# Performance work log

Hardware: AMD Instinct MI355X
Metric: run time of the kernel (lower is better)

Reference implementation:

```python
import jax, jax.numpy as jnp
import numpy as np

N_NODES = 100000


def _gcn_norm(edge_index, num_nodes):
    """Add self-loops and compute symmetric GCN normalization coefficients.
    Returns (src, dst, norm) for the augmented edge list."""
    loop = jnp.arange(num_nodes, dtype=edge_index.dtype)
    src = jnp.concatenate([edge_index[0], loop])
    dst = jnp.concatenate([edge_index[1], loop])
    deg = jax.ops.segment_sum(jnp.ones_like(src, dtype=jnp.float32), dst,
                              num_segments=num_nodes)
    dinv = jnp.where(deg > 0, jax.lax.rsqrt(deg), 0.0)
    norm = dinv[src] * dinv[dst]  # [E + N]
    return src, dst, norm


def setup_inputs() -> dict:
    key = jax.random.key(0)
    ks = jax.random.split(key, 7)
    d = 64
    E = 1000000
    x = jax.random.normal(ks[0], (N_NODES, d), dtype=jnp.float32)
    edge_index = jax.random.randint(ks[1], (2, E), 0, N_NODES, dtype=jnp.int64)
    s = 1.0 / np.sqrt(d)
    Ws = jax.random.normal(ks[2], (3, d, d), dtype=jnp.float32) * s
    bs = jax.random.normal(ks[3], (3, d), dtype=jnp.float32) * 0.02
    W_out = jax.random.normal(ks[4], (d, d), dtype=jnp.float32) * s
    b_out = jax.random.normal(ks[5], (d,), dtype=jnp.float32) * 0.02
    return {"x": x, "edge_index": edge_index, "Ws": Ws, "bs": bs,
            "W_out": W_out, "b_out": b_out}


def reference(x, edge_index, Ws, bs, W_out, b_out):
    num_nodes = x.shape[0]
    src, dst, norm = _gcn_norm(edge_index, num_nodes)  # fixed graph -> compute once
    for i in range(Ws.shape[0]):  # small fixed layer count
        h = x @ Ws[i]                              # [N, d] linear transform
        msg = norm[:, None] * h[src]               # gather + scale  [E+N, d]
        x = jax.ops.segment_sum(msg, dst, num_segments=num_nodes) + bs[i]
        x = jax.nn.relu(x)
    return x @ W_out + b_out
```

## Files before the change

### kernel.cpp

```cpp
#include <hip/hip_runtime.h>
#include <hip/hip_bf16.h>

#define D 64
#define BSHIFT 8
#define BNODES 256
#define BCAP 4096
#define PTILE 2048

typedef __attribute__((ext_vector_type(8))) short short8;
typedef __attribute__((ext_vector_type(4))) float float4v;


__device__ __forceinline__ float bf16u_to_f32(unsigned short u) {
  union { unsigned int i; float f; } c;
  c.i = ((unsigned int)u) << 16;
  return c.f;
}

__device__ __forceinline__ unsigned short f32_to_bf16u(float f) {
  union { float f; unsigned int u; } c;
  c.f = f;
  unsigned int r = (c.u + 0x7fffu + ((c.u >> 16) & 1u)) >> 16;
  return (unsigned short)r;
}


__global__ void k_probe(const void* W, const void* ei, int* flags) {
  int lane = threadIdx.x & 63;
  const unsigned short* wb = (const unsigned short*)W;
  bool big = false;
  for (int i = lane; i < 512; i += 64) {
    float v = bf16u_to_f32(wb[i]);
    if (!(fabsf(v) < 100.f)) big = true;
  }
  int anybig = __any(big);
  const int* e32 = (const int*)ei;
  bool nz = (e32[2 * lane + 1] != 0);
  int anynz = __any(nz);
  if (threadIdx.x == 0) {
    flags[0] = anybig ? 1 : 0;
    flags[1] = anynz ? 0 : 1;
  }
}


__global__ __launch_bounds__(256) void k_prep(
    const void* __restrict__ Ws, const void* __restrict__ Wout,
    const void* __restrict__ bs, const void* __restrict__ bout,
    const int* __restrict__ flags, unsigned short* __restrict__ WT,
    float* __restrict__ biasf, int* __restrict__ bucket_cursor) {
  int f32 = flags[0];
  int gid = blockIdx.x * 256 + threadIdx.x;
  int stride = gridDim.x * 256;

  for (int i = gid; i < 512; i += stride) bucket_cursor[i] = i * BCAP;

  for (int i = gid; i < 4 * 4096; i += stride) {
    int l = i >> 12;
    int r = i & 4095;
    int k = r >> 6;
    int nn = r & 63;
    unsigned short v;
    if (l < 3) {
      v = f32 ? f32_to_bf16u(((const float*)Ws)[l * 4096 + r])
              : ((const unsigned short*)Ws)[l * 4096 + r];
    } else {
      v = f32 ? f32_to_bf16u(((const float*)Wout)[r])
              : ((const unsigned short*)Wout)[r];
    }
    WT[l * 4096 + nn * 64 + k] = v;
  }
  for (int i = gid; i < 4 * 64; i += stride) {
    int l = i >> 6;
    int j = i & 63;
    float v;
    if (l < 3)
      v = f32 ? ((const float*)bs)[l * 64 + j]
              : bf16u_to_f32(((const unsigned short*)bs)[l * 64 + j]);
    else
      v = f32 ? ((const float*)bout)[j]
              : bf16u_to_f32(((const unsigned short*)bout)[j]);
    biasf[i] = v;
  }
}


__global__ __launch_bounds__(256) void k_partition(
    const void* __restrict__ ei, const int* __restrict__ flags,
    int* __restrict__ bucket_cursor, int* __restrict__ packed, int e) {
  __shared__ int lhist[512];
  __shared__ int lbase[512];
  int tid = threadIdx.x;
  int t0 = blockIdx.x * PTILE;
  int tend = min(t0 + PTILE, e);
  if (t0 >= e) return;
  int i64 = flags[1];

  for (int b = tid; b < 512; b += 256) lhist[b] = 0;
  __syncthreads();

  if (i64) {
    const long long* dst = (const long long*)ei + e;
    for (int i = t0 + tid; i < tend; i += 256)
      atomicAdd(&lhist[((int)dst[i]) >> BSHIFT], 1);
  } else {
    const int* dst = (const int*)ei + e;
    for (int i = t0 + tid; i < tend; i += 256)
      atomicAdd(&lhist[dst[i] >> BSHIFT], 1);
  }
  __syncthreads();

  for (int b = tid; b < 512; b += 256) {
    int c = lhist[b];
    lbase[b] = c ? atomicAdd(&bucket_cursor[b], c) : 0;
    lhist[b] = 0;
  }
  __syncthreads();

  if (i64) {
    const long long* srcp = (const long long*)ei;
    const long long* dstp = srcp + e;
    for (int i = t0 + tid; i < tend; i += 256) {
      int s = (int)srcp[i];
      int d = (int)dstp[i];
      int b = d >> BSHIFT;
      int r = atomicAdd(&lhist[b], 1);
      packed[lbase[b] + r] = (s << BSHIFT) | (d & (BNODES - 1));
    }
  } else {
    const int* srcp = (const int*)ei;
    const int* dstp = srcp + e;
    for (int i = t0 + tid; i < tend; i += 256) {
      int s = srcp[i];
      int d = dstp[i];
      int b = d >> BSHIFT;
      int r = atomicAdd(&lhist[b], 1);
      packed[lbase[b] + r] = (s << BSHIFT) | (d & (BNODES - 1));
    }
  }
}

__global__ __launch_bounds__(256) void k_sort_csr(
    const int* __restrict__ packed, const int* __restrict__ bucket_cursor,
    int* __restrict__ csr, int2* __restrict__ rowrange,
    float* __restrict__ dinv, int n) {
  __shared__ int lcnt[BNODES];
  __shared__ int lofs[BNODES];
  __shared__ int sbuf[BNODES];
  int tid = threadIdx.x;
  int bucket = blockIdx.x;
  int node0 = bucket << BSHIFT;
  int nodes = min(BNODES, n - node0);
  int s0 = bucket * BCAP;
  int s1 = bucket_cursor[bucket];
  lcnt[tid] = 0;
  __syncthreads();
  for (int i = s0 + tid; i < s1; i += 256)
    atomicAdd(&lcnt[packed[i] & (BNODES - 1)], 1);
  __syncthreads();
  int v = lcnt[tid];
  sbuf[tid] = v;
  __syncthreads();
  for (int off = 1; off < BNODES; off <<= 1) {
    int tv = (tid >= off) ? sbuf[tid - off] : 0;
    __syncthreads();
    sbuf[tid] += tv;
    __syncthreads();
  }
  int excl = sbuf[tid] - v;
  lofs[tid] = excl;
  lcnt[tid] = 0;
  if (tid < nodes) {
    rowrange[node0 + tid] = make_int2(s0 + excl, s0 + excl + v);
    dinv[node0 + tid] = rsqrtf((float)(v + 1));
  }
  __syncthreads();
  for (int i = s0 + tid; i < s1; i += 256) {
    int pk = packed[i];
    int ld = pk & (BNODES - 1);
    int r = atomicAdd(&lcnt[ld], 1);
    csr[s0 + lofs[ld] + r] = pk >> BSHIFT;
  }
}


__global__ __launch_bounds__(256) void k_scale(
    const void* __restrict__ x0, const int* __restrict__ flags,
    const float* __restrict__ dinv, ushort4* __restrict__ z, int n16) {
  int f32 = flags[0];
  int i = blockIdx.x * 256 + threadIdx.x;
  int stride = gridDim.x * 256;
  for (; i < n16; i += stride) {
    float d = dinv[i >> 4];
    ushort4 o;
    if (f32) {
      float4 v = ((const float4*)x0)[i];
      o.x = f32_to_bf16u(d * v.x);
      o.y = f32_to_bf16u(d * v.y);
      o.z = f32_to_bf16u(d * v.z);
      o.w = f32_to_bf16u(d * v.w);
    } else {
      ushort4 v = ((const ushort4*)x0)[i];
      o.x = f32_to_bf16u(d * bf16u_to_f32(v.x));
      o.y = f32_to_bf16u(d * bf16u_to_f32(v.y));
      o.z = f32_to_bf16u(d * bf16u_to_f32(v.z));
      o.w = f32_to_bf16u(d * bf16u_to_f32(v.w));
    }
    z[i] = o;
  }
}

__global__ __launch_bounds__(256, 4) void k_fused(
    const unsigned short* __restrict__ z, const int2* __restrict__ rowrange,
    const int* __restrict__ csr, const float* __restrict__ dinv,
    const unsigned short* __restrict__ WT, const float* __restrict__ biasf,
    unsigned short* __restrict__ out, int n, int scale_out) {
  __shared__ unsigned short ybf[16 * 80];
  int tid = threadIdx.x;
  int lane = tid & 63;
  int w = tid >> 6;
  int q = lane >> 4;
  int f = lane & 15;

  short8 b0 = *(const short8*)(WT + (size_t)(f + 16 * w) * 64 + q * 8);
  short8 b1 = *(const short8*)(WT + (size_t)(f + 16 * w) * 64 + 32 + q * 8);

  int row0 = blockIdx.x * 16;
  int base_node = row0 + w * 4;
  const ushort4* z4 = (const ushort4*)z;

  int2 rr[4];
#pragma unroll
  for (int j = 0; j < 4; j++) rr[j] = rowrange[base_node + j];

  float ac[4][4];
#pragma unroll
  for (int j = 0; j < 4; j++) {
    ushort4 sv = z4[(size_t)(base_node + j) * 16 + f];
    ac[j][0] = (q == 0) ? bf16u_to_f32(sv.x) : 0.f;
    ac[j][1] = (q == 0) ? bf16u_to_f32(sv.y) : 0.f;
    ac[j][2] = (q == 0) ? bf16u_to_f32(sv.z) : 0.f;
    ac[j][3] = (q == 0) ? bf16u_to_f32(sv.w) : 0.f;
  }

  int srcs[16];
  bool mm[16];
#pragma unroll
  for (int j = 0; j < 4; j++) {
#pragma unroll
    for (int u = 0; u < 4; u++) {
      int i = rr[j].x + 4 * u + q;
      bool m = i < rr[j].y;
      mm[j * 4 + u] = m;
      srcs[j * 4 + u] = csr[m ? i : rr[j].x];
    }
  }
  ushort4 g[16];
#pragma unroll
  for (int t = 0; t < 16; t++) g[t] = z4[(size_t)srcs[t] * 16 + f];
#pragma unroll
  for (int j = 0; j < 4; j++) {
#pragma unroll
    for (int u = 0; u < 4; u++) {
      ushort4 v = g[j * 4 + u];
      if (mm[j * 4 + u]) {
        ac[j][0] += bf16u_to_f32(v.x);
        ac[j][1] += bf16u_to_f32(v.y);
        ac[j][2] += bf16u_to_f32(v.z);
        ac[j][3] += bf16u_to_f32(v.w);
      }
    }
  }

#pragma unroll
  for (int j = 0; j < 4; j++) {
    for (int base = rr[j].x + 16; base < rr[j].y; base += 16) {
      int ts[4];
      bool tm[4];
#pragma unroll
      for (int u = 0; u < 4; u++) {
        int i = base + 4 * u + q;
        tm[u] = i < rr[j].y;
        ts[u] = csr[tm[u] ? i : rr[j].x];
      }
      ushort4 tv[4];
#pragma unroll
      for (int u = 0; u < 4; u++) tv[u] = z4[(size_t)ts[u] * 16 + f];
#pragma unroll
      for (int u = 0; u < 4; u++) {
        if (tm[u]) {
          ac[j][0] += bf16u_to_f32(tv[u].x);
          ac[j][1] += bf16u_to_f32(tv[u].y);
          ac[j][2] += bf16u_to_f32(tv[u].z);
          ac[j][3] += bf16u_to_f32(tv[u].w);
        }
      }
    }
  }

#pragma unroll
  for (int j = 0; j < 4; j++) {
#pragma unroll
    for (int c = 0; c < 4; c++) {
      ac[j][c] += __shfl_xor(ac[j][c], 16, 64);
      ac[j][c] += __shfl_xor(ac[j][c], 32, 64);
    }
  }
  if (q == 0) {
#pragma unroll
    for (int j = 0; j < 4; j++) {
      float dv = dinv[base_node + j];
      ushort4 o;
      o.x = f32_to_bf16u(dv * ac[j][0]);
      o.y = f32_to_bf16u(dv * ac[j][1]);
      o.z = f32_to_bf16u(dv * ac[j][2]);
      o.w = f32_to_bf16u(dv * ac[j][3]);
      *(ushort4*)&ybf[(w * 4 + j) * 80 + 4 * f] = o;
    }
  }
  __syncthreads();

  short8 a0 = *(const short8*)&ybf[f * 80 + q * 8];
  short8 a1 = *(const short8*)&ybf[f * 80 + 32 + q * 8];
  float4v zz = {0.f, 0.f, 0.f, 0.f};
  float4v acc = __builtin_amdgcn_mfma_f32_16x16x32_bf16(a0, b0, zz, 0, 0, 0);
  acc = __builtin_amdgcn_mfma_f32_16x16x32_bf16(a1, b1, acc, 0, 0, 0);

  float bv = biasf[16 * w + f];
  if (scale_out) {
    float4 dv4 = *(const float4*)(dinv + row0 + q * 4);
    float d[4] = {dv4.x, dv4.y, dv4.z, dv4.w};
#pragma unroll
    for (int reg = 0; reg < 4; reg++) {
      int row = row0 + q * 4 + reg;
      if (row < n)
        out[(size_t)row * 64 + 16 * w + f] =
            f32_to_bf16u(d[reg] * fmaxf(acc[reg] + bv, 0.f));
    }
  } else {
#pragma unroll
    for (int reg = 0; reg < 4; reg++) {
      int row = row0 + q * 4 + reg;
      if (row < n)
        out[(size_t)row * 64 + 16 * w + f] =
            f32_to_bf16u(fmaxf(acc[reg] + bv, 0.f));
    }
  }
}

__global__ __launch_bounds__(256) void k_gemm_final(
    const unsigned short* __restrict__ xin,
    const unsigned short* __restrict__ WT, const float* __restrict__ bias,
    void* __restrict__ out, const int* __restrict__ flags, int ntiles) {
  int lane = threadIdx.x & 63;
  int wid = threadIdx.x >> 6;
  int f = lane & 15;
  int q = lane >> 4;

  short8 bfr[4][2];
#pragma unroll
  for (int ct = 0; ct < 4; ct++)
#pragma unroll
    for (int kt = 0; kt < 2; kt++)
      bfr[ct][kt] =
          *(const short8*)(WT + (size_t)(f + 16 * ct) * 64 + kt * 32 + q * 8);

  int wave = blockIdx.x * 4 + wid;
  int nwaves = gridDim.x * 4;
  for (int t = wave; t < ntiles; t += nwaves) {
    int row0 = t * 16;
    const unsigned short* xr = xin + (size_t)(row0 + f) * 64 + q * 8;
    short8 a0 = *(const short8*)(xr);
    short8 a1 = *(const short8*)(xr + 32);
    float4v acc[4];
#pragma unroll
    for (int ct = 0; ct < 4; ct++) {
      float4v z = {0.f, 0.f, 0.f, 0.f};
      acc[ct] =
          __builtin_amdgcn_mfma_f32_16x16x32_bf16(a0, bfr[ct][0], z, 0, 0, 0);
      acc[ct] = __builtin_amdgcn_mfma_f32_16x16x32_bf16(a1, bfr[ct][1],
                                                        acc[ct], 0, 0, 0);
    }
    int f32o = flags[0];
    float bv[4];
#pragma unroll
    for (int ct = 0; ct < 4; ct++) bv[ct] = bias[f + 16 * ct];
    if (f32o) {
      float* op = (float*)out;
#pragma unroll
      for (int reg = 0; reg < 4; reg++) {
        size_t rb = (size_t)(row0 + q * 4 + reg) * 64 + f;
#pragma unroll
        for (int ct = 0; ct < 4; ct++) op[rb + 16 * ct] = acc[ct][reg] + bv[ct];
      }
    } else {
      unsigned short* op = (unsigned short*)out;
#pragma unroll
      for (int reg = 0; reg < 4; reg++) {
        size_t rb = (size_t)(row0 + q * 4 + reg) * 64 + f;
#pragma unroll
        for (int ct = 0; ct < 4; ct++)
          op[rb + 16 * ct] = f32_to_bf16u(acc[ct][reg] + bv[ct]);
      }
    }
  }
}


extern "C" void kernel_launch(void* const* d_in, const int* in_sizes, int n_in,
                              void* d_out, int out_size, void* d_ws,
                              size_t ws_size, hipStream_t stream) {
  const void* x0 = d_in[0];
  const void* ei = d_in[1];
  const void* Ws = d_in[2];
  const void* bs = d_in[3];
  const void* Wout = d_in[4];
  const void* bout = d_in[5];

  const int N = in_sizes[0] / D;
  const int E = in_sizes[1] / 2;
  const int NBUC = (N + BNODES - 1) >> BSHIFT;
  const int NT = (N + 15) / 16;

  char* p = (char*)d_ws;
  auto alloc = [&](size_t bytes) {
    char* r = p;
    p += (bytes + 511) & ~(size_t)511;
    return r;
  };
  int* flags = (int*)alloc(8);
  int* bucket_cursor = (int*)alloc(512 * 4);
  int* packed = (int*)alloc((size_t)512 * BCAP * 4);
  int* csr = (int*)alloc((size_t)512 * BCAP * 4);
  int2* rowrange = (int2*)alloc((size_t)N * 8);
  float* dinv = (float*)alloc((size_t)N * 4);
  unsigned short* WT = (unsigned short*)alloc(4 * 4096 * 2);
  float* biasf = (float*)alloc(4 * 64 * 4);
  unsigned short* za = (unsigned short*)alloc((size_t)N * D * 2);
  unsigned short* zb = (unsigned short*)alloc((size_t)N * D * 2);
  (void)ws_size;
  (void)n_in;
  (void)out_size;

  k_probe<<<1, 64, 0, stream>>>(Ws, ei, flags);
  k_prep<<<32, 256, 0, stream>>>(Ws, Wout, bs, bout, flags, WT, biasf,
                                 bucket_cursor);
  int ptiles = (E + PTILE - 1) / PTILE;
  k_partition<<<ptiles, 256, 0, stream>>>(ei, flags, bucket_cursor, packed, E);
  k_sort_csr<<<NBUC, 256, 0, stream>>>(packed, bucket_cursor, csr, rowrange,
                                       dinv, N);
  k_scale<<<1024, 256, 0, stream>>>(x0, flags, dinv, (ushort4*)za, N * 16);

  k_fused<<<NT, 256, 0, stream>>>(za, rowrange, csr, dinv, WT + 0 * 4096,
                                  biasf + 0 * 64, zb, N, 1);
  k_fused<<<NT, 256, 0, stream>>>(zb, rowrange, csr, dinv, WT + 1 * 4096,
                                  biasf + 1 * 64, za, N, 1);
  k_fused<<<NT, 256, 0, stream>>>(za, rowrange, csr, dinv, WT + 2 * 4096,
                                  biasf + 2 * 64, zb, N, 0);
  k_gemm_final<<<(NT + 3) / 4, 256, 0, stream>>>(zb, WT + 3 * 4096,
                                                 biasf + 3 * 64, d_out, flags,
                                                 NT);
}
```

Before: 264.7 us.

## Gather neighbor rows with 16-byte loads and shuffle-broadcast CSR indices

Reworks the fused gather-aggregate kernel so each lane loads 8 bf16 features (short8) rather than 4. Eight lanes now cover a 64-wide row, so each wave gathers 8 neighbors per instruction. Row ranges and CSR indices are loaded once per wave and broadcast with shuffles. The self-loop is folded into slot 0 of the first 16-entry batch. This is meant to cut the number of memory instructions and redundant index loads, at the cost of more registers (four 8-float accumulators) and a three-stage cross-lane reduction.

Measured after the change: 243.6 us. -8.0%, faster.

```diff
diff --git a/kernel.cpp b/kernel.cpp
--- a/kernel.cpp
+++ b/kernel.cpp
@@ -221,110 +221,123 @@
   int w = tid >> 6;
   int q = lane >> 4;
   int f = lane & 15;
+  int h = lane & 7;
+  int g8 = lane >> 3;
 
   short8 b0 = *(const short8*)(WT + (size_t)(f + 16 * w) * 64 + q * 8);
   short8 b1 = *(const short8*)(WT + (size_t)(f + 16 * w) * 64 + 32 + q * 8);
 
   int row0 = blockIdx.x * 16;
   int base_node = row0 + w * 4;
-  const ushort4* z4 = (const ushort4*)z;
-
-  int2 rr[4];
-#pragma unroll
-  for (int j = 0; j < 4; j++) rr[j] = rowrange[base_node + j];
-
-  float ac[4][4];
+  const short8* z8 = (const short8*)z;
+
+  int rrw = 0;
+  if (lane < 8) rrw = ((const int*)rowrange)[(size_t)base_node * 2 + lane];
+  int rx0 = __shfl(rrw, 0, 64);
+  int ry0 = __shfl(rrw, 1, 64);
+  int rx1 = __shfl(rrw, 2, 64);
+  int ry1 = __shfl(rrw, 3, 64);
+  int rx2 = __shfl(rrw, 4, 64);
+  int ry2 = __shfl(rrw, 5, 64);
+  int rx3 = __shfl(rrw, 6, 64);
+  int ry3 = __shfl(rrw, 7, 64);
+  int deg0 = ry0 - rx0;
+  int deg1 = ry1 - rx1;
+  int deg2 = ry2 - rx2;
+  int deg3 = ry3 - rx3;
+
+  int jx = lane >> 4;
+  int m = lane & 15;
+  int rxj = (jx & 2) ? ((jx & 1) ? rx3 : rx2) : ((jx & 1) ? rx1 : rx0);
+  int dgj = (jx & 2) ? ((jx & 1) ? deg3 : deg2) : ((jx & 1) ? deg1 : deg0);
+  int coff = (m >= 1 && m <= dgj) ? (m - 1) : 0;
+  int idx = csr[rxj + coff];
+  if (m == 0) idx = base_node + jx;
+
+  float ac[4][4][2];
+  float a0[8] = {0, 0, 0, 0, 0, 0, 0, 0};
+  float a1[8] = {0, 0, 0, 0, 0, 0, 0, 0};
+  float a2[8] = {0, 0, 0, 0, 0, 0, 0, 0};
+  float a3[8] = {0, 0, 0, 0, 0, 0, 0, 0};
+  (void)ac;
+
+  short8 g[8];
+#pragma unroll
+  for (int t = 0; t < 8; t++) {
+    int u = ((t & 1) << 3) + g8;
+    int sl = ((t >> 1) << 4) + u;
+    int s = __shfl(idx, sl, 64);
+    g[t] = z8[(size_t)s * 8 + h];
+  }
+#pragma unroll
+  for (int t = 0; t < 8; t++) {
+    int u = ((t & 1) << 3) + g8;
+    const int j = t >> 1;
+    int dg = (j == 0) ? deg0 : (j == 1) ? deg1 : (j == 2) ? deg2 : deg3;
+    float vm = (u <= dg) ? 1.f : 0.f;
+    float* aj = (j == 0) ? a0 : (j == 1) ? a1 : (j == 2) ? a2 : a3;
+#pragma unroll
+    for (int c = 0; c < 8; c++)
+      aj[c] += vm * bf16u_to_f32((unsigned short)g[t][c]);
+  }
+
 #pragma unroll
   for (int j = 0; j < 4; j++) {
-    ushort4 sv = z4[(size_t)(base_node + j) * 16 + f];
-    ac[j][0] = (q == 0) ? bf16u_to_f32(sv.x) : 0.f;
-    ac[j][1] = (q == 0) ? bf16u_to_f32(sv.y) : 0.f;
-    ac[j][2] = (q == 0) ? bf16u_to_f32(sv.z) : 0.f;
-    ac[j][3] = (q == 0) ? bf16u_to_f32(sv.w) : 0.f;
-  }
-
-  int srcs[16];
-  bool mm[16];
-#pragma unroll
-  for (int j = 0; j < 4; j++) {
-#pragma unroll
-    for (int u = 0; u < 4; u++) {
-      int i = rr[j].x + 4 * u + q;
-      bool m = i < rr[j].y;
-      mm[j * 4 + u] = m;
-      srcs[j * 4 + u] = csr[m ? i : rr[j].x];
-    }
-  }
-  ushort4 g[16];
-#pragma unroll
-  for (int t = 0; t < 16; t++) g[t] = z4[(size_t)srcs[t] * 16 + f];
-#pragma unroll
-  for (int j = 0; j < 4; j++) {
-#pragma unroll
-    for (int u = 0; u < 4; u++) {
-      ushort4 v = g[j * 4 + u];
-      if (mm[j * 4 + u]) {
-        ac[j][0] += bf16u_to_f32(v.x);
-        ac[j][1] += bf16u_to_f32(v.y);
-        ac[j][2] += bf16u_to_f32(v.z);
-        ac[j][3] += bf16u_to_f32(v.w);
-      }
-    }
-  }
-
-#pragma unroll
-  for (int j = 0; j < 4; j++) {
-    for (int base = rr[j].x + 16; base < rr[j].y; base += 16) {
-      int ts[4];
-      bool tm[4];
-#pragma unroll
-      for (int u = 0; u < 4; u++) {
-        int i = base + 4 * u + q;
-        tm[u] = i < rr[j].y;
-        ts[u] = csr[tm[u] ? i : rr[j].x];
-      }
-      ushort4 tv[4];
-#pragma unroll
-      for (int u = 0; u < 4; u++) tv[u] = z4[(size_t)ts[u] * 16 + f];
-#pragma unroll
-      for (int u = 0; u < 4; u++) {
-        if (tm[u]) {
-          ac[j][0] += bf16u_to_f32(tv[u].x);
-          ac[j][1] += bf16u_to_f32(tv[u].y);
-          ac[j][2] += bf16u_to_f32(tv[u].z);
-          ac[j][3] += bf16u_to_f32(tv[u].w);
-        }
-      }
-    }
-  }
-
-#pragma unroll
-  for (int j = 0; j < 4; j++) {
-#pragma unroll
-    for (int c = 0; c < 4; c++) {
-      ac[j][c] += __shfl_xor(ac[j][c], 16, 64);
-      ac[j][c] += __shfl_xor(ac[j][c], 32, 64);
-    }
-  }
-  if (q == 0) {
-#pragma unroll
-    for (int j = 0; j < 4; j++) {
-      float dv = dinv[base_node + j];
-      ushort4 o;
-      o.x = f32_to_bf16u(dv * ac[j][0]);
-      o.y = f32_to_bf16u(dv * ac[j][1]);
-      o.z = f32_to_bf16u(dv * ac[j][2]);
-      o.w = f32_to_bf16u(dv * ac[j][3]);
-      *(ushort4*)&ybf[(w * 4 + j) * 80 + 4 * f] = o;
-    }
-  }
-  __syncthreads();
-
-  short8 a0 = *(const short8*)&ybf[f * 80 + q * 8];
-  short8 a1 = *(const short8*)&ybf[f * 80 + 32 + q * 8];
+    int rx = (j == 0) ? rx0 : (j == 1) ? rx1 : (j == 2) ? rx2 : rx3;
+    int dg = (j == 0) ? deg0 : (j == 1) ? deg1 : (j == 2) ? deg2 : deg3;
+    float* aj = (j == 0) ? a0 : (j == 1) ? a1 : (j == 2) ? a2 : a3;
+    for (int e0 = 15; e0 < dg; e0 += 8) {
+      int e = e0 + g8;
+      bool vv = e < dg;
+      int s = csr[rx + (vv ? e : 0)];
+      short8 tv = z8[(size_t)s * 8 + h];
+      float vm = vv ? 1.f : 0.f;
+#pragma unroll
+      for (int c = 0; c < 8; c++)
+        aj[c] += vm * bf16u_to_f32((unsigned short)tv[c]);
+    }
+  }
+
+#pragma unroll
+  for (int c = 0; c < 8; c++) {
+    a0[c] += __shfl_xor(a0[c], 8, 64);
+    a1[c] += __shfl_xor(a1[c], 8, 64);
+    a2[c] += __shfl_xor(a2[c], 8, 64);
+    a3[c] += __shfl_xor(a3[c], 8, 64);
+    a0[c] += __shfl_xor(a0[c], 16, 64);
+    a1[c] += __shfl_xor(a1[c], 16, 64);
+    a2[c] += __shfl_xor(a2[c], 16, 64);
+    a3[c] += __shfl_xor(a3[c], 16, 64);
+    a0[c] += __shfl_xor(a0[c], 32, 64);
+    a1[c] += __shfl_xor(a1[c], 32, 64);
+    a2[c] += __shfl_xor(a2[c], 32, 64);
+    a3[c] += __shfl_xor(a3[c], 32, 64);
+  }
+
+  if (lane < 32) {
+    int jw = lane >> 3;
+    float dv = dinv[base_node + jw];
+    unsigned int pk[4];
+#pragma unroll
+    for (int cp = 0; cp < 4; cp++) {
+      float vlo = (jw & 2) ? ((jw & 1) ? a3[2 * cp] : a2[2 * cp])
+                           : ((jw & 1) ? a1[2 * cp] : a0[2 * cp]);
+      float vhi = (jw & 2) ? ((jw & 1) ? a3[2 * cp + 1] : a2[2 * cp + 1])
+                           : ((jw & 1) ? a1[2 * cp + 1] : a0[2 * cp + 1]);
+      unsigned int lo = f32_to_bf16u(dv * vlo);
+      unsigned int hi = f32_to_bf16u(dv * vhi);
+      pk[cp] = lo | (hi << 16);
+    }
+    *(uint4*)&ybf[(w * 4 + jw) * 80 + 8 * h] =
+        make_uint4(pk[0], pk[1], pk[2], pk[3]);
+  }
+  __syncthreads();
+
+  short8 fa0 = *(const short8*)&ybf[f * 80 + q * 8];
+  short8 fa1 = *(const short8*)&ybf[f * 80 + 32 + q * 8];
   float4v zz = {0.f, 0.f, 0.f, 0.f};
-  float4v acc = __builtin_amdgcn_mfma_f32_16x16x32_bf16(a0, b0, zz, 0, 0, 0);
-  acc = __builtin_amdgcn_mfma_f32_16x16x32_bf16(a1, b1, acc, 0, 0, 0);
+  float4v acc = __builtin_amdgcn_mfma_f32_16x16x32_bf16(fa0, b0, zz, 0, 0, 0);
+  acc = __builtin_amdgcn_mfma_f32_16x16x32_bf16(fa1, b1, acc, 0, 0, 0);
 
   float bv = biasf[16 * w + f];
   if (scale_out) {
```
